# Kernel optimization log

Measured on AMD Instinct MI355X. Metric: run time of the kernel, lower is better.

The kernel has to match this reference:

```python
import jax, jax.numpy as jnp
import numpy as np
import math

NB_FEATURES = 256

def _softmax_kernel(x, projection_matrix):
    # x: [B,H,N,D], projection_matrix: [D,F] -> [B,H,N,F]
    x_proj = jnp.einsum('bhnd,df->bhnf', x, projection_matrix)
    x_proj = x_proj - jnp.max(x_proj, axis=-1, keepdims=True)
    return jnp.exp(x_proj) / math.sqrt(projection_matrix.shape[-1])

def setup_inputs() -> dict:
    key = jax.random.key(0)
    k1, k2, k3, k4 = jax.random.split(key, 4)
    B, H, N, D = 2, 16, 4096, 64
    q = jax.random.normal(k1, (B, H, N, D), dtype=jnp.float32)
    k = jax.random.normal(k2, (B, H, N, D), dtype=jnp.float32)
    v = jax.random.normal(k3, (B, H, N, D), dtype=jnp.float32)
    projection_matrix = jax.random.normal(k4, (D, NB_FEATURES), dtype=jnp.float32)
    return {"q": q, "k": k, "v": v, "projection_matrix": projection_matrix}

def reference(q, k, v, projection_matrix):
    q_prime = _softmax_kernel(q, projection_matrix)  # [B,H,N,F]
    k_prime = _softmax_kernel(k, projection_matrix)  # [B,H,N,F]
    kv = jnp.einsum('bhnf,bhne->bhfe', k_prime, v)   # [B,H,F,E]
    denom = jnp.einsum('bhnf,bhf->bhn', q_prime, jnp.sum(k_prime, axis=-2) + 1e-06)
    z = 1.0 / denom[..., None]                        # [B,H,N,1]
    out = jnp.einsum('bhnf,bhfe->bhne', q_prime, kv)  # [B,H,N,E]
    return out * z
```

## Files before the change

kernel.cpp:

```cpp
#include <hip/hip_runtime.h>
#include <math.h>

typedef float f4 __attribute__((ext_vector_type(4)));
typedef float f32x4 __attribute__((ext_vector_type(4)));
typedef _Float16 h4 __attribute__((ext_vector_type(4)));
typedef _Float16 h8 __attribute__((ext_vector_type(8)));

#define BH 32
#define NN 4096
#define DD 64
#define FF 256
#define EE 64
#define SPLITS 8
#define ROWS_K (NN / SPLITS)
#define QB 8
#define ROWS_Q (NN / QB)
#define TILE 64
#define ST 72
#define STF 264

#define MFMA(a, b, c) __builtin_amdgcn_mfma_f32_16x16x32_f16((a), (b), (c), 0, 0, 0)

#define KVPART_F 4194304
#define KSPART_F 262144

__global__ __launch_bounds__(512, 2) void fa_kside(
    const float* __restrict__ kin, const float* __restrict__ vin,
    const float* __restrict__ P, float* __restrict__ kv_part,
    float* __restrict__ ksum_part) {
  __shared__ _Float16 Pt[FF * ST];
  __shared__ _Float16 kx[TILE * ST];
  __shared__ _Float16 vrow[TILE * ST];
  __shared__ _Float16 vt[TILE * ST];
  __shared__ _Float16 kpt[FF * ST];
  __shared__ float rowmax2[2][TILE];

  const int t = threadIdx.x;
  const int w = t >> 6, lane = t & 63;
  const int g = lane >> 4, fl = lane & 15;
  const int s = w & 3, nh = w >> 2;
  const int bh = blockIdx.x >> 3, split = blockIdx.x & 7;
  const int bhs = blockIdx.x;
  const int k0 = g * 8;

  {
    const f4* Pg4 = (const f4*)P;
#pragma unroll
    for (int i = 0; i < 8; ++i) {
      int idx = t + i * 512;
      f4 pv = Pg4[idx];
      int d = idx >> 6, f0 = (idx & 63) * 4;
      Pt[(f0 + 0) * ST + d] = (_Float16)pv.x;
      Pt[(f0 + 1) * ST + d] = (_Float16)pv.y;
      Pt[(f0 + 2) * ST + d] = (_Float16)pv.z;
      Pt[(f0 + 3) * ST + d] = (_Float16)pv.w;
    }
  }

  f32x4 kvacc[2][4];
#pragma unroll
  for (int mi = 0; mi < 2; ++mi)
#pragma unroll
    for (int nt = 0; nt < 4; ++nt) kvacc[mi][nt] = (f32x4){0.f, 0.f, 0.f, 0.f};
  float ksum_acc[8] = {0.f, 0.f, 0.f, 0.f, 0.f, 0.f, 0.f, 0.f};

  const size_t base = (size_t)bh * NN * DD + (size_t)split * ROWS_K * DD;

  for (int it = 0; it < ROWS_K / TILE; ++it) {
    const f4* kb4 = (const f4*)(kin + base + (size_t)it * TILE * DD);
    const f4* vb4 = (const f4*)(vin + base + (size_t)it * TILE * DD);
#pragma unroll
    for (int i = 0; i < 2; ++i) {
      int idx = t + i * 512;
      int r = idx >> 4, c4 = (idx & 15) * 4;
      f4 xv = kb4[idx];
      h4 hk;
      hk.x = (_Float16)xv.x; hk.y = (_Float16)xv.y;
      hk.z = (_Float16)xv.z; hk.w = (_Float16)xv.w;
      *(h4*)&kx[r * ST + c4] = hk;
      f4 vv = vb4[idx];
      h4 hv;
      hv.x = (_Float16)vv.x; hv.y = (_Float16)vv.y;
      hv.z = (_Float16)vv.z; hv.w = (_Float16)vv.w;
      *(h4*)&vrow[r * ST + c4] = hv;
    }
    __syncthreads();

    const int rA = s * 16 + fl;
    h8 a0 = *(const h8*)&kx[rA * ST + k0];
    h8 a1 = *(const h8*)&kx[rA * ST + 32 + k0];
    f32x4 lac[8];
#pragma unroll
    for (int T = 0; T < 8; ++T) {
      int ncol = (nh * 8 + T) * 16 + fl;
      h8 b0 = *(const h8*)&Pt[ncol * ST + k0];
      h8 b1 = *(const h8*)&Pt[ncol * ST + 32 + k0];
      f32x4 c = {0.f, 0.f, 0.f, 0.f};
      c = MFMA(a0, b0, c);
      c = MFMA(a1, b1, c);
      lac[T] = c;
    }

    {
      int e = lane, r0v = w * 8;
      h8 tv;
#pragma unroll
      for (int j = 0; j < 8; ++j) tv[j] = vrow[(r0v + j) * ST + e];
      *(h8*)&vt[e * ST + r0v] = tv;
    }

    {
      float mx[4];
#pragma unroll
      for (int rg = 0; rg < 4; ++rg) {
        float m = lac[0][rg];
#pragma unroll
        for (int T = 1; T < 8; ++T) m = fmaxf(m, lac[T][rg]);
#pragma unroll
        for (int off = 1; off <= 8; off <<= 1)
          m = fmaxf(m, __shfl_xor(m, off, 64));
        mx[rg] = m;
      }
      if (fl == 0) {
#pragma unroll
        for (int rg = 0; rg < 4; ++rg)
          rowmax2[nh][s * 16 + g * 4 + rg] = mx[rg];
      }
    }
    __syncthreads();

    {
      const int r0 = s * 16 + g * 4;
      float mrow[4];
#pragma unroll
      for (int rg = 0; rg < 4; ++rg)
        mrow[rg] = fmaxf(rowmax2[0][r0 + rg], rowmax2[1][r0 + rg]);
#pragma unroll
      for (int T = 0; T < 8; ++T) {
        int ncol = (nh * 8 + T) * 16 + fl;
        h4 kp;
#pragma unroll
        for (int rg = 0; rg < 4; ++rg) {
          float ev = __expf(lac[T][rg] - mrow[rg]) * 0.0625f;
          _Float16 hv = (_Float16)ev;
          ksum_acc[T] += (float)hv;
          kp[rg] = hv;
        }
        *(h4*)&kpt[ncol * ST + r0] = kp;
      }
    }
    __syncthreads();

    {
      h8 vb0[4], vb1[4];
#pragma unroll
      for (int nt = 0; nt < 4; ++nt) {
        int ec = nt * 16 + fl;
        vb0[nt] = *(const h8*)&vt[ec * ST + k0];
        vb1[nt] = *(const h8*)&vt[ec * ST + 32 + k0];
      }
#pragma unroll
      for (int mi = 0; mi < 2; ++mi) {
        int frow = (2 * w + mi) * 16 + fl;
        h8 ka0 = *(const h8*)&kpt[frow * ST + k0];
        h8 ka1 = *(const h8*)&kpt[frow * ST + 32 + k0];
#pragma unroll
        for (int nt = 0; nt < 4; ++nt) {
          kvacc[mi][nt] = MFMA(ka0, vb0[nt], kvacc[mi][nt]);
          kvacc[mi][nt] = MFMA(ka1, vb1[nt], kvacc[mi][nt]);
        }
      }
    }
  }

  float* kvp = kv_part + (size_t)bhs * (FF * EE);
#pragma unroll
  for (int mi = 0; mi < 2; ++mi)
#pragma unroll
    for (int nt = 0; nt < 4; ++nt)
#pragma unroll
      for (int rg = 0; rg < 4; ++rg) {
        int f = (2 * w + mi) * 16 + g * 4 + rg;
        int e = nt * 16 + fl;
        kvp[f * EE + e] = kvacc[mi][nt][rg];
      }

#pragma unroll
  for (int T = 0; T < 8; ++T) {
    float sg = ksum_acc[T];
    sg += __shfl_xor(sg, 16, 64);
    sg += __shfl_xor(sg, 32, 64);
    if (lane < 16)
      ksum_part[(size_t)bhs * 1024 + w * 128 + T * 16 + lane] = sg;
  }
}

__global__ __launch_bounds__(256) void fa_reduce(
    const float* __restrict__ kv_part, const float* __restrict__ ksum_part,
    _Float16* __restrict__ kvt_g, float* __restrict__ ksum_g) {
  __shared__ _Float16 lds[EE * STF];
  const int bh = blockIdx.x, t = threadIdx.x;
  for (int i = 0; i < 64; ++i) {
    int idx = i * 256 + t;
    int f = idx >> 6, e = idx & 63;
    float s = 0.f;
#pragma unroll
    for (int sp = 0; sp < SPLITS; ++sp)
      s += kv_part[(size_t)(bh * SPLITS + sp) * (FF * EE) + idx];
    lds[e * STF + f] = (_Float16)s;
  }
  {
    int f = t;
    float s = 0.f;
#pragma unroll
    for (int sp = 0; sp < SPLITS; ++sp)
#pragma unroll
      for (int j = 0; j < 4; ++j)
        s += ksum_part[(size_t)(bh * SPLITS + sp) * 1024 +
                       ((f >> 7) * 4 + j) * 128 + (f & 127)];
    ksum_g[bh * FF + f] = s + 1e-6f;
  }
  __syncthreads();
  unsigned int* og = (unsigned int*)kvt_g + (size_t)bh * 8192;
  for (int i = 0; i < 32; ++i) {
    int idx = i * 256 + t;
    int e = idx >> 7, fp = (idx & 127) * 2;
    og[idx] = *(const unsigned int*)&lds[e * STF + fp];
  }
}

__global__ __launch_bounds__(512, 2) void fa_qside(
    const float* __restrict__ qin, const float* __restrict__ P,
    const _Float16* __restrict__ kvt_g, const float* __restrict__ ksum_g,
    float* __restrict__ out) {
  __shared__ _Float16 Pt[FF * ST];
  __shared__ _Float16 qx[TILE * ST];
  __shared__ _Float16 qpt[TILE * STF];
  __shared__ _Float16 kvt[EE * STF];
  __shared__ float rowmax2[2][TILE];
  __shared__ float denp[2][TILE];

  const int t = threadIdx.x;
  const int w = t >> 6, lane = t & 63;
  const int g = lane >> 4, fl = lane & 15;
  const int s = w & 3, nh = w >> 2;
  const int bh = blockIdx.x >> 3, qb = blockIdx.x & 7;
  const int k0 = g * 8;

  {
    const f4* Pg4 = (const f4*)P;
#pragma unroll
    for (int i = 0; i < 8; ++i) {
      int idx = t + i * 512;
      f4 pv = Pg4[idx];
      int d = idx >> 6, f0 = (idx & 63) * 4;
      Pt[(f0 + 0) * ST + d] = (_Float16)pv.x;
      Pt[(f0 + 1) * ST + d] = (_Float16)pv.y;
      Pt[(f0 + 2) * ST + d] = (_Float16)pv.z;
      Pt[(f0 + 3) * ST + d] = (_Float16)pv.w;
    }
  }
  {
    const h8* src = (const h8*)(kvt_g + (size_t)bh * FF * EE);
#pragma unroll
    for (int i = 0; i < 4; ++i) {
      int idx = t + i * 512;
      int e = idx >> 5, f0 = (idx & 31) * 8;
      *(h8*)&kvt[e * STF + f0] = src[idx];
    }
  }
  float ksr[8];
#pragma unroll
  for (int T = 0; T < 8; ++T)
    ksr[T] = ksum_g[bh * FF + nh * 128 + T * 16 + fl];

  const size_t base = (size_t)bh * NN * DD + (size_t)qb * ROWS_Q * DD;
  float* ob = out + (size_t)bh * NN * EE + (size_t)qb * ROWS_Q * EE;

  for (int it = 0; it < ROWS_Q / TILE; ++it) {
    const f4* qb4 = (const f4*)(qin + base + (size_t)it * TILE * DD);
#pragma unroll
    for (int i = 0; i < 2; ++i) {
      int idx = t + i * 512;
      int r = idx >> 4, c4 = (idx & 15) * 4;
      f4 xv = qb4[idx];
      h4 hq;
      hq.x = (_Float16)xv.x; hq.y = (_Float16)xv.y;
      hq.z = (_Float16)xv.z; hq.w = (_Float16)xv.w;
      *(h4*)&qx[r * ST + c4] = hq;
    }
    __syncthreads();

    const int rA = s * 16 + fl;
    h8 a0 = *(const h8*)&qx[rA * ST + k0];
    h8 a1 = *(const h8*)&qx[rA * ST + 32 + k0];
    f32x4 lac[8];
#pragma unroll
    for (int T = 0; T < 8; ++T) {
      int ncol = (nh * 8 + T) * 16 + fl;
      h8 b0 = *(const h8*)&Pt[ncol * ST + k0];
      h8 b1 = *(const h8*)&Pt[ncol * ST + 32 + k0];
      f32x4 c = {0.f, 0.f, 0.f, 0.f};
      c = MFMA(a0, b0, c);
      c = MFMA(a1, b1, c);
      lac[T] = c;
    }
    {
      float mx[4];
#pragma unroll
      for (int rg = 0; rg < 4; ++rg) {
        float m = lac[0][rg];
#pragma unroll
        for (int T = 1; T < 8; ++T) m = fmaxf(m, lac[T][rg]);
#pragma unroll
        for (int off = 1; off <= 8; off <<= 1)
          m = fmaxf(m, __shfl_xor(m, off, 64));
        mx[rg] = m;
      }
      if (fl == 0) {
#pragma unroll
        for (int rg = 0; rg < 4; ++rg)
          rowmax2[nh][s * 16 + g * 4 + rg] = mx[rg];
      }
    }
    __syncthreads();

    {
      const int r0 = s * 16 + g * 4;
      float mrow[4];
#pragma unroll
      for (int rg = 0; rg < 4; ++rg)
        mrow[rg] = fmaxf(rowmax2[0][r0 + rg], rowmax2[1][r0 + rg]);
      float den[4] = {0.f, 0.f, 0.f, 0.f};
#pragma unroll
      for (int T = 0; T < 8; ++T) {
        int ncol = (nh * 8 + T) * 16 + fl;
#pragma unroll
        for (int rg = 0; rg < 4; ++rg) {
          float ev = __expf(lac[T][rg] - mrow[rg]) * 0.0625f;
          _Float16 hv = (_Float16)ev;
          den[rg] += (float)hv * ksr[T];
          qpt[(r0 + rg) * STF + ncol] = hv;
        }
      }
#pragma unroll
      for (int rg = 0; rg < 4; ++rg) {
#pragma unroll
        for (int off = 1; off <= 8; off <<= 1)
          den[rg] += __shfl_xor(den[rg], off, 64);
      }
      if (fl == 0) {
#pragma unroll
        for (int rg = 0; rg < 4; ++rg) denp[nh][r0 + rg] = den[rg];
      }
    }
    __syncthreads();

    {
      f32x4 oacc[2];
      oacc[0] = (f32x4){0.f, 0.f, 0.f, 0.f};
      oacc[1] = (f32x4){0.f, 0.f, 0.f, 0.f};
      const int row = s * 16 + fl;
#pragma unroll
      for (int kst = 0; kst < 8; ++kst) {
        h8 aq = *(const h8*)&qpt[row * STF + kst * 32 + k0];
#pragma unroll
        for (int ni = 0; ni < 2; ++ni) {
          int ec = (nh * 2 + ni) * 16 + fl;
          h8 bq = *(const h8*)&kvt[ec * STF + kst * 32 + k0];
          oacc[ni] = MFMA(aq, bq, oacc[ni]);
        }
      }
      const int r0 = s * 16 + g * 4;
      float* obt = ob + (size_t)it * TILE * EE;
#pragma unroll
      for (int rg = 0; rg < 4; ++rg) {
        int ro = r0 + rg;
        float dn = denp[0][ro] + denp[1][ro];
        float inv = 1.0f / dn;
#pragma unroll
        for (int ni = 0; ni < 2; ++ni) {
          int e = (nh * 2 + ni) * 16 + fl;
          obt[ro * EE + e] = oacc[ni][rg] * inv;
        }
      }
    }
  }
}

extern "C" void kernel_launch(void* const* d_in, const int* in_sizes, int n_in,
                              void* d_out, int out_size, void* d_ws,
                              size_t ws_size, hipStream_t stream) {
  (void)in_sizes;
  (void)n_in;
  (void)out_size;
  (void)ws_size;
  const float* q = (const float*)d_in[0];
  const float* k = (const float*)d_in[1];
  const float* v = (const float*)d_in[2];
  const float* P = (const float*)d_in[3];
  float* out = (float*)d_out;

  float* kv_part = (float*)d_ws;
  float* ksum_part = kv_part + KVPART_F;
  _Float16* kvt_g = (_Float16*)(ksum_part + KSPART_F);
  float* ksum_g = (float*)(kvt_g + BH * FF * EE);

  hipLaunchKernelGGL(fa_kside, dim3(BH * SPLITS), dim3(512), 0, stream, k, v, P,
                     kv_part, ksum_part);
  hipLaunchKernelGGL(fa_reduce, dim3(BH), dim3(256), 0, stream, kv_part,
                     ksum_part, kvt_g, ksum_g);
  hipLaunchKernelGGL(fa_qside, dim3(BH * QB), dim3(512), 0, stream, q, P, kvt_g,
                     ksum_g, out);
}
```

Measured before the change: 199.2 us.

## Restructure k/q kernels so each wave owns full rows; parallelize reduce

Each wave now computes all 256 features for its own 16 rows, so the row max is a wave-local shuffle reduction. This removes the cross-wave rowmax and denominator LDS exchanges and several barriers per tile. Inputs are loaded straight from global memory into MFMA fragments, with no LDS staging of k and q. The k-side processes 128-row tiles with a larger kpt/vt buffer, and ksum partials are pre-reduced in LDS. fa_reduce now runs on 544 blocks instead of 32, trading extra launch width for more parallelism. The changes raise register pressure (16 accumulator tiles per wave) and use uncoalesced strided global loads for V.

```diff
diff --git a/kernel.cpp b/kernel.cpp
--- a/kernel.cpp
+++ b/kernel.cpp
@@ -12,33 +12,36 @@
 #define FF 256
 #define EE 64
 #define SPLITS 8
-#define ROWS_K (NN / SPLITS)
+#define ROWS_K 512
 #define QB 8
-#define ROWS_Q (NN / QB)
-#define TILE 64
+#define ROWS_Q 512
 #define ST 72
+#define SK 136
 #define STF 264
 
 #define MFMA(a, b, c) __builtin_amdgcn_mfma_f32_16x16x32_f16((a), (b), (c), 0, 0, 0)
 
-#define KVPART_F 4194304
-#define KSPART_F 262144
+__device__ inline h8 cvt2(f4 x0, f4 x1) {
+  h8 r;
+  r[0] = (_Float16)x0.x; r[1] = (_Float16)x0.y;
+  r[2] = (_Float16)x0.z; r[3] = (_Float16)x0.w;
+  r[4] = (_Float16)x1.x; r[5] = (_Float16)x1.y;
+  r[6] = (_Float16)x1.z; r[7] = (_Float16)x1.w;
+  return r;
+}
 
 __global__ __launch_bounds__(512, 2) void fa_kside(
     const float* __restrict__ kin, const float* __restrict__ vin,
     const float* __restrict__ P, float* __restrict__ kv_part,
     float* __restrict__ ksum_part) {
   __shared__ _Float16 Pt[FF * ST];
-  __shared__ _Float16 kx[TILE * ST];
-  __shared__ _Float16 vrow[TILE * ST];
-  __shared__ _Float16 vt[TILE * ST];
-  __shared__ _Float16 kpt[FF * ST];
-  __shared__ float rowmax2[2][TILE];
+  __shared__ _Float16 kpt[FF * SK];
+  __shared__ _Float16 vt[EE * SK];
+  __shared__ float ks_lds[8 * FF];
 
   const int t = threadIdx.x;
   const int w = t >> 6, lane = t & 63;
   const int g = lane >> 4, fl = lane & 15;
-  const int s = w & 3, nh = w >> 2;
   const int bh = blockIdx.x >> 3, split = blockIdx.x & 7;
   const int bhs = blockIdx.x;
   const int k0 = g * 8;
@@ -62,37 +65,36 @@
   for (int mi = 0; mi < 2; ++mi)
 #pragma unroll
     for (int nt = 0; nt < 4; ++nt) kvacc[mi][nt] = (f32x4){0.f, 0.f, 0.f, 0.f};
-  float ksum_acc[8] = {0.f, 0.f, 0.f, 0.f, 0.f, 0.f, 0.f, 0.f};
+  float ksum_acc[16];
+#pragma unroll
+  for (int T = 0; T < 16; ++T) ksum_acc[T] = 0.f;
 
   const size_t base = (size_t)bh * NN * DD + (size_t)split * ROWS_K * DD;
-
-  for (int it = 0; it < ROWS_K / TILE; ++it) {
-    const f4* kb4 = (const f4*)(kin + base + (size_t)it * TILE * DD);
-    const f4* vb4 = (const f4*)(vin + base + (size_t)it * TILE * DD);
-#pragma unroll
-    for (int i = 0; i < 2; ++i) {
-      int idx = t + i * 512;
-      int r = idx >> 4, c4 = (idx & 15) * 4;
-      f4 xv = kb4[idx];
-      h4 hk;
-      hk.x = (_Float16)xv.x; hk.y = (_Float16)xv.y;
-      hk.z = (_Float16)xv.z; hk.w = (_Float16)xv.w;
-      *(h4*)&kx[r * ST + c4] = hk;
-      f4 vv = vb4[idx];
-      h4 hv;
-      hv.x = (_Float16)vv.x; hv.y = (_Float16)vv.y;
-      hv.z = (_Float16)vv.z; hv.w = (_Float16)vv.w;
-      *(h4*)&vrow[r * ST + c4] = hv;
-    }
-    __syncthreads();
-
-    const int rA = s * 16 + fl;
-    h8 a0 = *(const h8*)&kx[rA * ST + k0];
-    h8 a1 = *(const h8*)&kx[rA * ST + 32 + k0];
-    f32x4 lac[8];
-#pragma unroll
-    for (int T = 0; T < 8; ++T) {
-      int ncol = (nh * 8 + T) * 16 + fl;
+  __syncthreads();
+
+  for (int tile = 0; tile < 4; ++tile) {
+    if (tile) __syncthreads();
+    const int r0g = tile * 128 + w * 16;
+
+    const float* krow = kin + base + (size_t)(r0g + fl) * DD;
+    h8 a0 = cvt2(*(const f4*)&krow[k0], *(const f4*)&krow[k0 + 4]);
+    h8 a1 = cvt2(*(const f4*)&krow[32 + k0], *(const f4*)&krow[32 + k0 + 4]);
+
+    {
+      const float* vb = vin + base + (size_t)r0g * DD + lane;
+      h8 tv0, tv1;
+#pragma unroll
+      for (int j = 0; j < 8; ++j) tv0[j] = (_Float16)vb[j * DD];
+#pragma unroll
+      for (int j = 0; j < 8; ++j) tv1[j] = (_Float16)vb[(8 + j) * DD];
+      *(h8*)&vt[lane * SK + w * 16] = tv0;
+      *(h8*)&vt[lane * SK + w * 16 + 8] = tv1;
+    }
+
+    f32x4 lac[16];
+#pragma unroll
+    for (int T = 0; T < 16; ++T) {
+      int ncol = T * 16 + fl;
       h8 b0 = *(const h8*)&Pt[ncol * ST + k0];
       h8 b1 = *(const h8*)&Pt[ncol * ST + 32 + k0];
       f32x4 c = {0.f, 0.f, 0.f, 0.f};
@@ -101,74 +103,45 @@
       lac[T] = c;
     }
 
-    {
-      int e = lane, r0v = w * 8;
-      h8 tv;
-#pragma unroll
-      for (int j = 0; j < 8; ++j) tv[j] = vrow[(r0v + j) * ST + e];
-      *(h8*)&vt[e * ST + r0v] = tv;
-    }
-
-    {
-      float mx[4];
+    float mrow[4];
+#pragma unroll
+    for (int rg = 0; rg < 4; ++rg) {
+      float m = lac[0][rg];
+#pragma unroll
+      for (int T = 1; T < 16; ++T) m = fmaxf(m, lac[T][rg]);
+#pragma unroll
+      for (int off = 1; off <= 8; off <<= 1)
+        m = fmaxf(m, __shfl_xor(m, off, 64));
+      mrow[rg] = m;
+    }
+
+#pragma unroll
+    for (int T = 0; T < 16; ++T) {
+      int ncol = T * 16 + fl;
+      h4 kp;
 #pragma unroll
       for (int rg = 0; rg < 4; ++rg) {
-        float m = lac[0][rg];
-#pragma unroll
-        for (int T = 1; T < 8; ++T) m = fmaxf(m, lac[T][rg]);
-#pragma unroll
-        for (int off = 1; off <= 8; off <<= 1)
-          m = fmaxf(m, __shfl_xor(m, off, 64));
-        mx[rg] = m;
-      }
-      if (fl == 0) {
-#pragma unroll
-        for (int rg = 0; rg < 4; ++rg)
-          rowmax2[nh][s * 16 + g * 4 + rg] = mx[rg];
-      }
+        float ev = __expf(lac[T][rg] - mrow[rg]) * 0.0625f;
+        _Float16 hv = (_Float16)ev;
+        ksum_acc[T] += (float)hv;
+        kp[rg] = hv;
+      }
+      *(h4*)&kpt[ncol * SK + w * 16 + g * 4] = kp;
     }
     __syncthreads();
 
-    {
-      const int r0 = s * 16 + g * 4;
-      float mrow[4];
-#pragma unroll
-      for (int rg = 0; rg < 4; ++rg)
-        mrow[rg] = fmaxf(rowmax2[0][r0 + rg], rowmax2[1][r0 + rg]);
-#pragma unroll
-      for (int T = 0; T < 8; ++T) {
-        int ncol = (nh * 8 + T) * 16 + fl;
-        h4 kp;
-#pragma unroll
-        for (int rg = 0; rg < 4; ++rg) {
-          float ev = __expf(lac[T][rg] - mrow[rg]) * 0.0625f;
-          _Float16 hv = (_Float16)ev;
-          ksum_acc[T] += (float)hv;
-          kp[rg] = hv;
-        }
-        *(h4*)&kpt[ncol * ST + r0] = kp;
-      }
-    }
-    __syncthreads();
-
-    {
-      h8 vb0[4], vb1[4];
-#pragma unroll
-      for (int nt = 0; nt < 4; ++nt) {
-        int ec = nt * 16 + fl;
-        vb0[nt] = *(const h8*)&vt[ec * ST + k0];
-        vb1[nt] = *(const h8*)&vt[ec * ST + 32 + k0];
-      }
+#pragma unroll
+    for (int kst = 0; kst < 4; ++kst) {
+      h8 vbf[4];
+#pragma unroll
+      for (int nt = 0; nt < 4; ++nt)
+        vbf[nt] = *(const h8*)&vt[(nt * 16 + fl) * SK + kst * 32 + k0];
 #pragma unroll
       for (int mi = 0; mi < 2; ++mi) {
-        int frow = (2 * w + mi) * 16 + fl;
-        h8 ka0 = *(const h8*)&kpt[frow * ST + k0];
-        h8 ka1 = *(const h8*)&kpt[frow * ST + 32 + k0];
-#pragma unroll
-        for (int nt = 0; nt < 4; ++nt) {
-          kvacc[mi][nt] = MFMA(ka0, vb0[nt], kvacc[mi][nt]);
-          kvacc[mi][nt] = MFMA(ka1, vb1[nt], kvacc[mi][nt]);
-        }
+        h8 ka = *(const h8*)&kpt[((2 * w + mi) * 16 + fl) * SK + kst * 32 + k0];
+#pragma unroll
+        for (int nt = 0; nt < 4; ++nt)
+          kvacc[mi][nt] = MFMA(ka, vbf[nt], kvacc[mi][nt]);
       }
     }
   }
@@ -186,46 +159,53 @@
       }
 
 #pragma unroll
-  for (int T = 0; T < 8; ++T) {
-    float sg = ksum_acc[T];
-    sg += __shfl_xor(sg, 16, 64);
-    sg += __shfl_xor(sg, 32, 64);
-    if (lane < 16)
-      ksum_part[(size_t)bhs * 1024 + w * 128 + T * 16 + lane] = sg;
+  for (int T = 0; T < 16; ++T) {
+    float s = ksum_acc[T];
+    s += __shfl_xor(s, 16, 64);
+    s += __shfl_xor(s, 32, 64);
+    if (lane < 16) ks_lds[w * FF + T * 16 + lane] = s;
+  }
+  __syncthreads();
+  if (t < FF) {
+    float s = 0.f;
+#pragma unroll
+    for (int wi = 0; wi < 8; ++wi) s += ks_lds[wi * FF + t];
+    ksum_part[(size_t)bhs * FF + t] = s;
   }
 }
 
 __global__ __launch_bounds__(256) void fa_reduce(
     const float* __restrict__ kv_part, const float* __restrict__ ksum_part,
     _Float16* __restrict__ kvt_g, float* __restrict__ ksum_g) {
-  __shared__ _Float16 lds[EE * STF];
-  const int bh = blockIdx.x, t = threadIdx.x;
-  for (int i = 0; i < 64; ++i) {
-    int idx = i * 256 + t;
-    int f = idx >> 6, e = idx & 63;
+  __shared__ _Float16 tl[EE * 18];
+  const int b = blockIdx.x, t = threadIdx.x;
+  if (b < 512) {
+    const int bh = b >> 4, c = b & 15;
+#pragma unroll
+    for (int i = 0; i < 4; ++i) {
+      int idx = i * 256 + t;
+      int fr = idx >> 6, e = idx & 63;
+      float s = 0.f;
+#pragma unroll
+      for (int sp = 0; sp < SPLITS; ++sp)
+        s += kv_part[(size_t)(bh * SPLITS + sp) * (FF * EE) + (c * 16 + fr) * EE + e];
+      tl[e * 18 + fr] = (_Float16)s;
+    }
+    __syncthreads();
+    unsigned int* og = (unsigned int*)kvt_g + (size_t)bh * 8192;
+#pragma unroll
+    for (int i = 0; i < 2; ++i) {
+      int idx = i * 256 + t;
+      int e = idx >> 3, fp = (idx & 7) * 2;
+      og[e * 128 + c * 8 + (idx & 7)] = *(unsigned int*)&tl[e * 18 + fp];
+    }
+  } else {
+    const int bh = b - 512;
     float s = 0.f;
 #pragma unroll
     for (int sp = 0; sp < SPLITS; ++sp)
-      s += kv_part[(size_t)(bh * SPLITS + sp) * (FF * EE) + idx];
-    lds[e * STF + f] = (_Float16)s;
-  }
-  {
-    int f = t;
-    float s = 0.f;
-#pragma unroll
-    for (int sp = 0; sp < SPLITS; ++sp)
-#pragma unroll
-      for (int j = 0; j < 4; ++j)
-        s += ksum_part[(size_t)(bh * SPLITS + sp) * 1024 +
-                       ((f >> 7) * 4 + j) * 128 + (f & 127)];
-    ksum_g[bh * FF + f] = s + 1e-6f;
-  }
-  __syncthreads();
-  unsigned int* og = (unsigned int*)kvt_g + (size_t)bh * 8192;
-  for (int i = 0; i < 32; ++i) {
-    int idx = i * 256 + t;
-    int e = idx >> 7, fp = (idx & 127) * 2;
-    og[idx] = *(const unsigned int*)&lds[e * STF + fp];
+      s += ksum_part[(size_t)(bh * SPLITS + sp) * FF + t];
+    ksum_g[bh * FF + t] = s + 1e-6f;
   }
 }
 
@@ -234,16 +214,12 @@
     const _Float16* __restrict__ kvt_g, const float* __restrict__ ksum_g,
     float* __restrict__ out) {
   __shared__ _Float16 Pt[FF * ST];
-  __shared__ _Float16 qx[TILE * ST];
-  __shared__ _Float16 qpt[TILE * STF];
   __shared__ _Float16 kvt[EE * STF];
-  __shared__ float rowmax2[2][TILE];
-  __shared__ float denp[2][TILE];
+  __shared__ _Float16 qpt[8 * 16 * STF];
 
   const int t = threadIdx.x;
   const int w = t >> 6, lane = t & 63;
   const int g = lane >> 4, fl = lane & 15;
-  const int s = w & 3, nh = w >> 2;
   const int bh = blockIdx.x >> 3, qb = blockIdx.x & 7;
   const int k0 = g * 8;
 
@@ -269,35 +245,25 @@
       *(h8*)&kvt[e * STF + f0] = src[idx];
     }
   }
-  float ksr[8];
-#pragma unroll
-  for (int T = 0; T < 8; ++T)
-    ksr[T] = ksum_g[bh * FF + nh * 128 + T * 16 + fl];
-
+  float ksr[16];
+#pragma unroll
+  for (int T = 0; T < 16; ++T) ksr[T] = ksum_g[bh * FF + T * 16 + fl];
+  __syncthreads();
+
+  _Float16* myqpt = qpt + w * 16 * STF;
   const size_t base = (size_t)bh * NN * DD + (size_t)qb * ROWS_Q * DD;
   float* ob = out + (size_t)bh * NN * EE + (size_t)qb * ROWS_Q * EE;
 
-  for (int it = 0; it < ROWS_Q / TILE; ++it) {
-    const f4* qb4 = (const f4*)(qin + base + (size_t)it * TILE * DD);
-#pragma unroll
-    for (int i = 0; i < 2; ++i) {
-      int idx = t + i * 512;
-      int r = idx >> 4, c4 = (idx & 15) * 4;
-      f4 xv = qb4[idx];
-      h4 hq;
-      hq.x = (_Float16)xv.x; hq.y = (_Float16)xv.y;
-      hq.z = (_Float16)xv.z; hq.w = (_Float16)xv.w;
-      *(h4*)&qx[r * ST + c4] = hq;
-    }
-    __syncthreads();
-
-    const int rA = s * 16 + fl;
-    h8 a0 = *(const h8*)&qx[rA * ST + k0];
-    h8 a1 = *(const h8*)&qx[rA * ST + 32 + k0];
-    f32x4 lac[8];
-#pragma unroll
-    for (int T = 0; T < 8; ++T) {
-      int ncol = (nh * 8 + T) * 16 + fl;
+  for (int st = 0; st < 4; ++st) {
+    const int r0g = st * 128 + w * 16;
+    const float* qrow = qin + base + (size_t)(r0g + fl) * DD;
+    h8 a0 = cvt2(*(const f4*)&qrow[k0], *(const f4*)&qrow[k0 + 4]);
+    h8 a1 = cvt2(*(const f4*)&qrow[32 + k0], *(const f4*)&qrow[32 + k0 + 4]);
+
+    f32x4 lac[16];
+#pragma unroll
+    for (int T = 0; T < 16; ++T) {
+      int ncol = T * 16 + fl;
       h8 b0 = *(const h8*)&Pt[ncol * ST + k0];
       h8 b1 = *(const h8*)&Pt[ncol * ST + 32 + k0];
       f32x4 c = {0.f, 0.f, 0.f, 0.f};
@@ -305,84 +271,59 @@
       c = MFMA(a1, b1, c);
       lac[T] = c;
     }
-    {
-      float mx[4];
+
+    float mrow[4];
+#pragma unroll
+    for (int rg = 0; rg < 4; ++rg) {
+      float m = lac[0][rg];
+#pragma unroll
+      for (int T = 1; T < 16; ++T) m = fmaxf(m, lac[T][rg]);
+#pragma unroll
+      for (int off = 1; off <= 8; off <<= 1)
+        m = fmaxf(m, __shfl_xor(m, off, 64));
+      mrow[rg] = m;
+    }
+
+    float den[4] = {0.f, 0.f, 0.f, 0.f};
+#pragma unroll
+    for (int T = 0; T < 16; ++T) {
+      int ncol = T * 16 + fl;
 #pragma unroll
       for (int rg = 0; rg < 4; ++rg) {
-        float m = lac[0][rg];
-#pragma unroll
-        for (int T = 1; T < 8; ++T) m = fmaxf(m, lac[T][rg]);
-#pragma unroll
-        for (int off = 1; off <= 8; off <<= 1)
-          m = fmaxf(m, __shfl_xor(m, off, 64));
-        mx[rg] = m;
-      }
-      if (fl == 0) {
-#pragma unroll
-        for (int rg = 0; rg < 4; ++rg)
-          rowmax2[nh][s * 16 + g * 4 + rg] = mx[rg];
-      }
-    }
-    __syncthreads();
-
-    {
-      const int r0 = s * 16 + g * 4;
-      float mrow[4];
-#pragma unroll
-      for (int rg = 0; rg < 4; ++rg)
-        mrow[rg] = fmaxf(rowmax2[0][r0 + rg], rowmax2[1][r0 + rg]);
-      float den[4] = {0.f, 0.f, 0.f, 0.f};
-#pragma unroll
-      for (int T = 0; T < 8; ++T) {
-        int ncol = (nh * 8 + T) * 16 + fl;
-#pragma unroll
-        for (int rg = 0; rg < 4; ++rg) {
-          float ev = __expf(lac[T][rg] - mrow[rg]) * 0.0625f;
-          _Float16 hv = (_Float16)ev;
-          den[rg] += (float)hv * ksr[T];
-          qpt[(r0 + rg) * STF + ncol] = hv;
-        }
-      }
-#pragma unroll
-      for (int rg = 0; rg < 4; ++rg) {
-#pragma unroll
-        for (int off = 1; off <= 8; off <<= 1)
-          den[rg] += __shfl_xor(den[rg], off, 64);
-      }
-      if (fl == 0) {
-#pragma unroll
-        for (int rg = 0; rg < 4; ++rg) denp[nh][r0 + rg] = den[rg];
-      }
-    }
-    __syncthreads();
-
-    {
-      f32x4 oacc[2];
-      oacc[0] = (f32x4){0.f, 0.f, 0.f, 0.f};
-      oacc[1] = (f32x4){0.f, 0.f, 0.f, 0.f};
-      const int row = s * 16 + fl;
-#pragma unroll
-      for (int kst = 0; kst < 8; ++kst) {
-        h8 aq = *(const h8*)&qpt[row * STF + kst * 32 + k0];
-#pragma unroll
-        for (int ni = 0; ni < 2; ++ni) {
-          int ec = (nh * 2 + ni) * 16 + fl;
-          h8 bq = *(const h8*)&kvt[ec * STF + kst * 32 + k0];
-          oacc[ni] = MFMA(aq, bq, oacc[ni]);
-        }
-      }
-      const int r0 = s * 16 + g * 4;
-      float* obt = ob + (size_t)it * TILE * EE;
-#pragma unroll
-      for (int rg = 0; rg < 4; ++rg) {
-        int ro = r0 + rg;
-        float dn = denp[0][ro] + denp[1][ro];
-        float inv = 1.0f / dn;
-#pragma unroll
-        for (int ni = 0; ni < 2; ++ni) {
-          int e = (nh * 2 + ni) * 16 + fl;
-          obt[ro * EE + e] = oacc[ni][rg] * inv;
-        }
+        float ev = __expf(lac[T][rg] - mrow[rg]) * 0.0625f;
+        _Float16 hv = (_Float16)ev;
+        den[rg] += (float)hv * ksr[T];
+        myqpt[(g * 4 + rg) * STF + ncol] = hv;
+      }
+    }
+#pragma unroll
+    for (int rg = 0; rg < 4; ++rg) {
+#pragma unroll
+      for (int off = 1; off <= 8; off <<= 1)
+        den[rg] += __shfl_xor(den[rg], off, 64);
+    }
+
+    f32x4 oacc[4];
+#pragma unroll
+    for (int nt = 0; nt < 4; ++nt) oacc[nt] = (f32x4){0.f, 0.f, 0.f, 0.f};
+#pragma unroll
+    for (int kst = 0; kst < 8; ++kst) {
+      h8 aq = *(const h8*)&myqpt[fl * STF + kst * 32 + k0];
+#pragma unroll
+      for (int nt = 0; nt < 4; ++nt) {
+        h8 bq = *(const h8*)&kvt[(nt * 16 + fl) * STF + kst * 32 + k0];
+        oacc[nt] = MFMA(aq, bq, oacc[nt]);
+      }
+    }
+
+    float* obt = ob + (size_t)r0g * EE;
+#pragma unroll
+    for (int rg = 0; rg < 4; ++rg) {
+      float inv = 1.0f / den[rg];
+#pragma unroll
+      for (int nt = 0; nt < 4; ++nt) {
+        int e = nt * 16 + fl;
+        obt[(g * 4 + rg) * EE + e] = oacc[nt][rg] * inv;
       }
     }
   }
@@ -402,13 +343,13 @@
   float* out = (float*)d_out;
 
   float* kv_part = (float*)d_ws;
-  float* ksum_part = kv_part + KVPART_F;
-  _Float16* kvt_g = (_Float16*)(ksum_part + KSPART_F);
-  float* ksum_g = (float*)(kvt_g + BH * FF * EE);
+  float* ksum_part = kv_part + 256 * 16384;
+  _Float16* kvt_g = (_Float16*)(ksum_part + 256 * 256);
+  float* ksum_g = (float*)(kvt_g + 32 * 16384);
 
   hipLaunchKernelGGL(fa_kside, dim3(BH * SPLITS), dim3(512), 0, stream, k, v, P,
                      kv_part, ksum_part);
-  hipLaunchKernelGGL(fa_reduce, dim3(BH), dim3(256), 0, stream, kv_part,
+  hipLaunchKernelGGL(fa_reduce, dim3(544), dim3(256), 0, stream, kv_part,
                      ksum_part, kvt_g, ksum_g);
   hipLaunchKernelGGL(fa_qside, dim3(BH * QB), dim3(512), 0, stream, q, P, kvt_g,
                      ksum_g, out);
```

New measurement: 176.0 us. 11.6% less time.
